# Kernel optimization log

Measured on AMD Instinct MI355X. Metric: run time of the kernel, lower is better.

The kernel has to match this reference:

```python
import jax, jax.numpy as jnp
import numpy as np

B, T, C = 4, 2048, 1024
N_HEAD = 16
HEAD_DIM = C // N_HEAD

def setup_inputs() -> dict:
    key = jax.random.key(0)
    k1, k2, k3, k4, k5 = jax.random.split(key, 5)
    sigma = (1.0 / C) ** 0.5  # encoder_var=1 default
    return {
        "x": jax.random.normal(k1, (B, T, C), dtype=jnp.float32),
        "W_attn": jax.random.normal(k2, (3 * C, C), dtype=jnp.float32) * sigma,
        "b_attn": jax.random.normal(k3, (3 * C,), dtype=jnp.float32),
        "W_proj": jax.random.normal(k4, (C, C), dtype=jnp.float32) * sigma,
        "b_proj": jax.random.normal(k5, (C,), dtype=jnp.float32),
    }

def reference(x, W_attn, b_attn, W_proj, b_proj):
    Bq, Tq, Cq = x.shape
    qkv = x @ W_attn.T + b_attn              # [B,T,3C]
    q, k, v = jnp.split(qkv, 3, axis=-1)
    def to_heads(t):
        return t.reshape(Bq, Tq, N_HEAD, HEAD_DIM).transpose(0, 2, 1, 3)  # [B,H,T,D]
    q, k, v = to_heads(q), to_heads(k), to_heads(v)
    # NOTE: original scales by 1/head_dim (not 1/sqrt(head_dim))
    att = jnp.einsum('bhqd,bhkd->bhqk', q, k) * (1.0 / HEAD_DIM)
    causal = jnp.tril(jnp.ones((Tq, Tq), dtype=bool))
    att = jnp.where(causal[None, None], att, -jnp.inf)
    att = jax.nn.softmax(att, axis=-1)
    y = jnp.einsum('bhqk,bhkd->bhqd', att, v)
    y = y.transpose(0, 2, 1, 3).reshape(Bq, Tq, Cq)
    return y @ W_proj.T + b_proj
```

## Files before the change

kernel.cpp:

```cpp
#include <hip/hip_runtime.h>

typedef __attribute__((ext_vector_type(8))) short s16x8;
typedef __attribute__((ext_vector_type(4))) float f32x4;
typedef __attribute__((ext_vector_type(4))) unsigned short u16x4;

#define T_  2048
#define C_  1024
#define D_  64

__device__ __forceinline__ unsigned short f2bf(float f){
  union { float fv; unsigned int u; } v; v.fv = f;
  unsigned int r = v.u + 0x7FFFu + ((v.u >> 16) & 1u);
  return (unsigned short)(r >> 16);
}

__device__ __forceinline__ float exp2_asm(float x){
  float r; asm("v_exp_f32 %0, %1" : "=v"(r) : "v"(x)); return r;
}
__device__ __forceinline__ unsigned int cvtpk(float lo, float hi){
  unsigned int r; asm("v_cvt_pk_bf16_f32 %0, %1, %2" : "=v"(r) : "v"(lo), "v"(hi)); return r;
}

__device__ __forceinline__ void gload_lds16(const void* g, void* l){
  __builtin_amdgcn_global_load_lds(
      (const __attribute__((address_space(1))) unsigned int*)g,
      (__attribute__((address_space(3))) unsigned int*)l, 16, 0, 0);
}

__global__ __launch_bounds__(256) void cvt_kernel(const float* __restrict__ src,
                                                  unsigned short* __restrict__ dst){
  size_t i = ((size_t)blockIdx.x * 256u + threadIdx.x) * 8u;
  f32x4 a = *(const f32x4*)(src + i);
  f32x4 b = *(const f32x4*)(src + i + 4);
  s16x8 o;
  #pragma unroll
  for (int j = 0; j < 4; ++j){ o[j] = (short)f2bf(a[j]); o[4+j] = (short)f2bf(b[j]); }
  *(s16x8*)(dst + i) = o;
}

template<int MODE>
__global__ __launch_bounds__(256, 2) void gemm_bt(
    const unsigned short* __restrict__ A, const unsigned short* __restrict__ Bw,
    const float* __restrict__ bias, int M, int N, int K, int nbx,
    unsigned short* __restrict__ q_ws, unsigned short* __restrict__ k_ws,
    unsigned short* __restrict__ vT_ws, float* __restrict__ out)
{
  __shared__ unsigned short Asm[2][128*64];
  __shared__ unsigned short Bsm[2][128*64];
  const int tid = threadIdx.x;
  const int lane = tid & 63, wid = tid >> 6;
  const int g = lane >> 4, lr = lane & 15;
  const int wr = wid >> 1, wc = wid & 1;
  const int nwg = (int)gridDim.x;
  const int cpx = nwg >> 3;
  const int orig = (int)blockIdx.x;
  const int wgid = (orig & 7) * cpx + (orig >> 3);
  const int bx = wgid % nbx, by = wgid / nbx;
  const int m0 = by * 128, n0 = bx * 128;
  const int swz = (lr & 7) << 4;

  f32x4 acc[4][4];
  #pragma unroll
  for (int i = 0; i < 4; ++i)
    #pragma unroll
    for (int j = 0; j < 4; ++j) acc[i][j] = (f32x4){0.f,0.f,0.f,0.f};

  auto stage = [&](int kt, int buf){
    const int k0 = kt << 6;
    #pragma unroll
    for (int j = 0; j < 4; ++j){
      const int c = j*256 + tid;
      const int row = c >> 3, jc = c & 7;
      const int sc = (jc ^ (row & 7)) << 4;
      gload_lds16((const char*)A  + ((size_t)(m0+row)*K + k0)*2 + sc,
                  (char*)&Asm[buf][0] + (size_t)c*16);
      gload_lds16((const char*)Bw + ((size_t)(n0+row)*K + k0)*2 + sc,
                  (char*)&Bsm[buf][0] + (size_t)c*16);
    }
  };

  const int nk = K >> 6;
  stage(0, 0);
  stage(1, 1);

  for (int t = 0; t < nk; ++t){
    const int cur = t & 1;
    if (t < nk - 1) asm volatile("s_waitcnt vmcnt(8)" ::: "memory");
    else            asm volatile("s_waitcnt vmcnt(0)" ::: "memory");
    asm volatile("s_barrier" ::: "memory");

    const char* At = (const char*)&Asm[cur][0];
    const char* Bt = (const char*)&Bsm[cur][0];

    #pragma unroll
    for (int s = 0; s < 2; ++s){
      s16x8 af[4], bf[4];
      #pragma unroll
      for (int mi = 0; mi < 4; ++mi){
        const int row = wr*64 + mi*16 + lr;
        af[mi] = *(const s16x8*)(At + row*128 + ((s*64 + g*16) ^ swz));
      }
      #pragma unroll
      for (int ni = 0; ni < 4; ++ni){
        const int row = wc*64 + ni*16 + lr;
        bf[ni] = *(const s16x8*)(Bt + row*128 + ((s*64 + g*16) ^ swz));
      }
      __builtin_amdgcn_s_setprio(1);
      #pragma unroll
      for (int mi = 0; mi < 4; ++mi)
        #pragma unroll
        for (int ni = 0; ni < 4; ++ni)
          acc[mi][ni] = __builtin_amdgcn_mfma_f32_16x16x32_bf16(af[mi], bf[ni], acc[mi][ni], 0, 0, 0);
      __builtin_amdgcn_s_setprio(0);
    }

    asm volatile("s_barrier" ::: "memory");
    if (t + 2 < nk) stage(t + 2, cur);
  }

  #pragma unroll
  for (int mi = 0; mi < 4; ++mi){
    #pragma unroll
    for (int ni = 0; ni < 4; ++ni){
      const int n = n0 + wc*64 + ni*16 + lr;
      const float bv = bias[n];
      #pragma unroll
      for (int r = 0; r < 4; ++r){
        const int m = m0 + wr*64 + mi*16 + g*4 + r;
        const float val = acc[mi][ni][r] + bv;
        if (MODE == 0){
          const int which = n >> 10;
          const int cc = n & 1023;
          const int h = cc >> 6, d = cc & 63;
          const int bq = m >> 11, t = m & 2047;
          const int bh = bq*16 + h;
          if (which == 0)      q_ws[((size_t)bh*T_ + t)*D_ + d] = f2bf(val * 0.022542110013890054f);
          else if (which == 1) k_ws[((size_t)bh*T_ + t)*D_ + d] = f2bf(val);
          else                 vT_ws[((size_t)bh*D_ + d)*T_ + t] = f2bf(val);
        } else {
          out[(size_t)m*N + n] = val;
        }
      }
    }
  }
}

__global__ __launch_bounds__(256, 4) void attn_kernel(
    const unsigned short* __restrict__ q_ws, const unsigned short* __restrict__ k_ws,
    const unsigned short* __restrict__ vT_ws, unsigned short* __restrict__ y_ws)
{
  __shared__ __align__(16) unsigned short Ks[2][64*64];
  __shared__ __align__(16) unsigned short Vs[2][64*64];

  const int tid = threadIdx.x;
  const int lane = tid & 63, wid = tid >> 6;
  const int g = lane >> 4, lr = lane & 15;
  const int orig = (int)blockIdx.x;
  const int wgid = (orig & 7) * 128 + (orig >> 3);
  const int p  = wgid & 15;
  const int bh = wgid >> 4;
  const int qwA = p*64 + wid*16,  qwB = (31 - p)*64 + wid*16;
  const int qrowA = qwA + lr,     qrowB = qwB + lr;
  const int swz = (lr & 7) << 4;

  const unsigned short* Qb = q_ws  + (size_t)bh*T_*D_;
  const unsigned short* Kb = k_ws  + (size_t)bh*T_*D_;
  const unsigned short* Vb = vT_ws + (size_t)bh*D_*T_;

  auto stage = [&](int t, int buf){
    const int kt0 = t << 6;
    #pragma unroll
    for (int s = 0; s < 2; ++s){
      const int c = s*256 + tid;
      const int r = c >> 3;
      const int scol = ((c & 7) << 4) ^ ((r & 7) << 4);
      gload_lds16((const char*)Kb + ((size_t)(kt0 + r)*D_)*2 + scol,
                  (char*)&Ks[buf][0] + c*16);
      gload_lds16((const char*)Vb + ((size_t)r*T_ + kt0)*2 + scol,
                  (char*)&Vs[buf][0] + c*16);
    }
  };

  const s16x8 bqA0 = *(const s16x8*)&Qb[(size_t)(qwA+lr)*D_ + g*8];
  const s16x8 bqA1 = *(const s16x8*)&Qb[(size_t)(qwA+lr)*D_ + 32 + g*8];
  const s16x8 bqB0 = *(const s16x8*)&Qb[(size_t)(qwB+lr)*D_ + g*8];
  const s16x8 bqB1 = *(const s16x8*)&Qb[(size_t)(qwB+lr)*D_ + 32 + g*8];

  s16x8 ones;
  #pragma unroll
  for (int j = 0; j < 8; ++j) ones[j] = (short)0x3F80;

  f32x4 yA[4], yB[4];
  #pragma unroll
  for (int dt = 0; dt < 4; ++dt){ yA[dt] = (f32x4){0.f,0.f,0.f,0.f}; yB[dt] = (f32x4){0.f,0.f,0.f,0.f}; }
  f32x4 lacA = (f32x4){0.f,0.f,0.f,0.f}, lacB = (f32x4){0.f,0.f,0.f,0.f};
  float mA = -1e30f, mB = -1e30f;

  const int ntA = p + 1, ntB = 32 - p;
  stage(0, 0);
  __syncthreads();

  for (int t = 0; t < ntB; ++t){
    const int cur = t & 1;
    if (t + 1 < ntB) stage(t + 1, cur ^ 1);
    const int kt0 = t << 6;
    const unsigned short* Kt = &Ks[cur][0];
    const unsigned short* Vt = &Vs[cur][0];
    unsigned short* Pw = &Ks[cur][wid*1024];
    const bool actA = (t < ntA);

    f32x4 sB[4], sA[4];
    #pragma unroll
    for (int kk = 0; kk < 4; ++kk){
      const int row = kk*16 + lr;
      const s16x8 a0 = *(const s16x8*)&Kt[row*64 + (((g*16)      ^ swz) >> 1)];
      const s16x8 a1 = *(const s16x8*)&Kt[row*64 + (((64 + g*16) ^ swz) >> 1)];
      f32x4 acc = (f32x4){0.f,0.f,0.f,0.f};
      acc = __builtin_amdgcn_mfma_f32_16x16x32_bf16(a0, bqB0, acc, 0, 0, 0);
      acc = __builtin_amdgcn_mfma_f32_16x16x32_bf16(a1, bqB1, acc, 0, 0, 0);
      sB[kk] = acc;
      if (actA){
        f32x4 acc2 = (f32x4){0.f,0.f,0.f,0.f};
        acc2 = __builtin_amdgcn_mfma_f32_16x16x32_bf16(a0, bqA0, acc2, 0, 0, 0);
        acc2 = __builtin_amdgcn_mfma_f32_16x16x32_bf16(a1, bqA1, acc2, 0, 0, 0);
        sA[kk] = acc2;
      }
    }

    if (kt0 + 63 > qwB){
      #pragma unroll
      for (int kk = 0; kk < 4; ++kk)
        #pragma unroll
        for (int r = 0; r < 4; ++r)
          if (kt0 + kk*16 + g*4 + r > qrowB) sB[kk][r] = -1e30f;
    }
    {
      float m01 = fmaxf(fmaxf(sB[0][0], sB[0][1]), fmaxf(sB[0][2], sB[0][3]));
      float m23 = fmaxf(fmaxf(sB[1][0], sB[1][1]), fmaxf(sB[1][2], sB[1][3]));
      float m45 = fmaxf(fmaxf(sB[2][0], sB[2][1]), fmaxf(sB[2][2], sB[2][3]));
      float m67 = fmaxf(fmaxf(sB[3][0], sB[3][1]), fmaxf(sB[3][2], sB[3][3]));
      float mx = fmaxf(fmaxf(m01, m23), fmaxf(m45, m67));
      mx = fmaxf(mx, __shfl_xor(mx, 16, 64));
      mx = fmaxf(mx, __shfl_xor(mx, 32, 64));
      if (!__all(mx <= mB + 8.f)){
        const float mnew = fmaxf(mB, mx);
        const float corr = exp2_asm(mB - mnew);
        mB = mnew;
        lacB[0] *= corr;
        #pragma unroll
        for (int dt = 0; dt < 4; ++dt)
          #pragma unroll
          for (int r = 0; r < 4; ++r) yB[dt][r] *= corr;
      }
    }
    union { unsigned int u[2]; u16x4 v; } pkB[4];
    #pragma unroll
    for (int kk = 0; kk < 4; ++kk){
      const float e0 = exp2_asm(sB[kk][0] - mB);
      const float e1 = exp2_asm(sB[kk][1] - mB);
      const float e2 = exp2_asm(sB[kk][2] - mB);
      const float e3 = exp2_asm(sB[kk][3] - mB);
      pkB[kk].u[0] = cvtpk(e0, e1);
      pkB[kk].u[1] = cvtpk(e2, e3);
    }

    asm volatile("s_barrier" ::: "memory");

    #pragma unroll
    for (int kk = 0; kk < 4; ++kk)
      *(u16x4*)&Pw[lr*64 + (((kk*32 + g*8) ^ swz) >> 1)] = pkB[kk].v;
    asm volatile("" ::: "memory");
    {
      const s16x8 p0 = *(const s16x8*)&Pw[lr*64 + (((g*16)      ^ swz) >> 1)];
      const s16x8 p1 = *(const s16x8*)&Pw[lr*64 + (((64 + g*16) ^ swz) >> 1)];
      lacB = __builtin_amdgcn_mfma_f32_16x16x32_bf16(ones, p0, lacB, 0, 0, 0);
      lacB = __builtin_amdgcn_mfma_f32_16x16x32_bf16(ones, p1, lacB, 0, 0, 0);
      #pragma unroll
      for (int dt = 0; dt < 4; ++dt){
        const int vrow = dt*16 + lr;
        const s16x8 v0 = *(const s16x8*)&Vt[vrow*64 + (((g*16)      ^ swz) >> 1)];
        const s16x8 v1 = *(const s16x8*)&Vt[vrow*64 + (((64 + g*16) ^ swz) >> 1)];
        yB[dt] = __builtin_amdgcn_mfma_f32_16x16x32_bf16(v0, p0, yB[dt], 0, 0, 0);
        yB[dt] = __builtin_amdgcn_mfma_f32_16x16x32_bf16(v1, p1, yB[dt], 0, 0, 0);
      }
    }

    if (actA){
      if (kt0 + 63 > qwA){
        #pragma unroll
        for (int kk = 0; kk < 4; ++kk)
          #pragma unroll
          for (int r = 0; r < 4; ++r)
            if (kt0 + kk*16 + g*4 + r > qrowA) sA[kk][r] = -1e30f;
      }
      float m01 = fmaxf(fmaxf(sA[0][0], sA[0][1]), fmaxf(sA[0][2], sA[0][3]));
      float m23 = fmaxf(fmaxf(sA[1][0], sA[1][1]), fmaxf(sA[1][2], sA[1][3]));
      float m45 = fmaxf(fmaxf(sA[2][0], sA[2][1]), fmaxf(sA[2][2], sA[2][3]));
      float m67 = fmaxf(fmaxf(sA[3][0], sA[3][1]), fmaxf(sA[3][2], sA[3][3]));
      float mx = fmaxf(fmaxf(m01, m23), fmaxf(m45, m67));
      mx = fmaxf(mx, __shfl_xor(mx, 16, 64));
      mx = fmaxf(mx, __shfl_xor(mx, 32, 64));
      if (!__all(mx <= mA + 8.f)){
        const float mnew = fmaxf(mA, mx);
        const float corr = exp2_asm(mA - mnew);
        mA = mnew;
        lacA[0] *= corr;
        #pragma unroll
        for (int dt = 0; dt < 4; ++dt)
          #pragma unroll
          for (int r = 0; r < 4; ++r) yA[dt][r] *= corr;
      }
      union { unsigned int u[2]; u16x4 v; } pkA[4];
      #pragma unroll
      for (int kk = 0; kk < 4; ++kk){
        const float e0 = exp2_asm(sA[kk][0] - mA);
        const float e1 = exp2_asm(sA[kk][1] - mA);
        const float e2 = exp2_asm(sA[kk][2] - mA);
        const float e3 = exp2_asm(sA[kk][3] - mA);
        pkA[kk].u[0] = cvtpk(e0, e1);
        pkA[kk].u[1] = cvtpk(e2, e3);
      }
      asm volatile("" ::: "memory");
      #pragma unroll
      for (int kk = 0; kk < 4; ++kk)
        *(u16x4*)&Pw[lr*64 + (((kk*32 + g*8) ^ swz) >> 1)] = pkA[kk].v;
      asm volatile("" ::: "memory");
      const s16x8 p0 = *(const s16x8*)&Pw[lr*64 + (((g*16)      ^ swz) >> 1)];
      const s16x8 p1 = *(const s16x8*)&Pw[lr*64 + (((64 + g*16) ^ swz) >> 1)];
      lacA = __builtin_amdgcn_mfma_f32_16x16x32_bf16(ones, p0, lacA, 0, 0, 0);
      lacA = __builtin_amdgcn_mfma_f32_16x16x32_bf16(ones, p1, lacA, 0, 0, 0);
      #pragma unroll
      for (int dt = 0; dt < 4; ++dt){
        const int vrow = dt*16 + lr;
        const s16x8 v0 = *(const s16x8*)&Vt[vrow*64 + (((g*16)      ^ swz) >> 1)];
        const s16x8 v1 = *(const s16x8*)&Vt[vrow*64 + (((64 + g*16) ^ swz) >> 1)];
        yA[dt] = __builtin_amdgcn_mfma_f32_16x16x32_bf16(v0, p0, yA[dt], 0, 0, 0);
        yA[dt] = __builtin_amdgcn_mfma_f32_16x16x32_bf16(v1, p1, yA[dt], 0, 0, 0);
      }
    }

    __syncthreads();
  }

  const int bq = bh >> 4, h = bh & 15;
  {
    const float inv = 1.f / lacB[0];
    #pragma unroll
    for (int dt = 0; dt < 4; ++dt){
      union { unsigned int u[2]; u16x4 v; } w;
      w.u[0] = cvtpk(yB[dt][0]*inv, yB[dt][1]*inv);
      w.u[1] = cvtpk(yB[dt][2]*inv, yB[dt][3]*inv);
      *(u16x4*)&y_ws[((size_t)(bq*T_ + qwB + lr))*C_ + h*64 + dt*16 + g*4] = w.v;
    }
  }
  {
    const float inv = 1.f / lacA[0];
    #pragma unroll
    for (int dt = 0; dt < 4; ++dt){
      union { unsigned int u[2]; u16x4 v; } w;
      w.u[0] = cvtpk(yA[dt][0]*inv, yA[dt][1]*inv);
      w.u[1] = cvtpk(yA[dt][2]*inv, yA[dt][3]*inv);
      *(u16x4*)&y_ws[((size_t)(bq*T_ + qwA + lr))*C_ + h*64 + dt*16 + g*4] = w.v;
    }
  }
}

extern "C" void kernel_launch(void* const* d_in, const int* in_sizes, int n_in,
                              void* d_out, int out_size, void* d_ws, size_t ws_size,
                              hipStream_t stream) {
  const float* x  = (const float*)d_in[0];
  const float* Wa = (const float*)d_in[1];
  const float* ba = (const float*)d_in[2];
  const float* Wp = (const float*)d_in[3];
  const float* bp = (const float*)d_in[4];
  float* out = (float*)d_out;

  char* ws = (char*)d_ws;
  const size_t MB = 1024u*1024u;
  unsigned short* xb  = (unsigned short*)(ws + 0);
  unsigned short* wab = (unsigned short*)(ws + 16*MB);
  unsigned short* wpb = (unsigned short*)(ws + 22*MB);
  unsigned short* qws = (unsigned short*)(ws + 24*MB);
  unsigned short* kws = (unsigned short*)(ws + 40*MB);
  unsigned short* vT  = (unsigned short*)(ws + 56*MB);
  unsigned short* yws = (unsigned short*)(ws + 72*MB);

  cvt_kernel<<<4096, 256, 0, stream>>>(x,  xb);
  cvt_kernel<<<1536, 256, 0, stream>>>(Wa, wab);
  cvt_kernel<<< 512, 256, 0, stream>>>(Wp, wpb);

  gemm_bt<0><<<dim3(1536), 256, 0, stream>>>(xb, wab, ba, 8192, 3072, 1024, 24,
                                             qws, kws, vT, nullptr);
  attn_kernel<<<dim3(1024), 256, 0, stream>>>(qws, kws, vT, yws);
  gemm_bt<1><<<dim3(512), 256, 0, stream>>>(yws, wpb, bp, 8192, 1024, 1024, 8,
                                            nullptr, nullptr, nullptr, out);
}
```

Before: 195.0 us.

## Restructure GEMM into 256x128 tiles with 4-slot K=32 pipeline

The GEMM now runs 8-wave workgroups over 256x128 output tiles. Each wave still computes 64x64, and B fragments are shared across more waves. The K loop is split into 32-wide steps held in a 4-slot LDS ring with 3 stages in flight, a rotating swizzle, and a single barrier per step, with global loads issued before the MFMAs. The goal is to hide memory latency better and cut barrier overhead. In exchange there are more loop iterations with fewer MFMAs each, and fewer workgroups in the grid.

```diff
diff --git a/kernel.cpp b/kernel.cpp
--- a/kernel.cpp
+++ b/kernel.cpp
@@ -39,25 +39,24 @@
 }
 
 template<int MODE>
-__global__ __launch_bounds__(256, 2) void gemm_bt(
+__global__ __launch_bounds__(512, 2) void gemm_bt(
     const unsigned short* __restrict__ A, const unsigned short* __restrict__ Bw,
     const float* __restrict__ bias, int M, int N, int K, int nbx,
     unsigned short* __restrict__ q_ws, unsigned short* __restrict__ k_ws,
     unsigned short* __restrict__ vT_ws, float* __restrict__ out)
 {
-  __shared__ unsigned short Asm[2][128*64];
-  __shared__ unsigned short Bsm[2][128*64];
+  __shared__ unsigned short Asl[4][256*32];
+  __shared__ unsigned short Bsl[4][128*32];
   const int tid = threadIdx.x;
   const int lane = tid & 63, wid = tid >> 6;
   const int g = lane >> 4, lr = lane & 15;
-  const int wr = wid >> 1, wc = wid & 1;
+  const int wm = wid >> 1, wn = wid & 1;
   const int nwg = (int)gridDim.x;
   const int cpx = nwg >> 3;
   const int orig = (int)blockIdx.x;
   const int wgid = (orig & 7) * cpx + (orig >> 3);
   const int bx = wgid % nbx, by = wgid / nbx;
-  const int m0 = by * 128, n0 = bx * 128;
-  const int swz = (lr & 7) << 4;
+  const int m0 = by * 256, n0 = bx * 128;
 
   f32x4 acc[4][4];
   #pragma unroll
@@ -65,68 +64,80 @@
     #pragma unroll
     for (int j = 0; j < 4; ++j) acc[i][j] = (f32x4){0.f,0.f,0.f,0.f};
 
-  auto stage = [&](int kt, int buf){
-    const int k0 = kt << 6;
-    #pragma unroll
-    for (int j = 0; j < 4; ++j){
-      const int c = j*256 + tid;
-      const int row = c >> 3, jc = c & 7;
-      const int sc = (jc ^ (row & 7)) << 4;
-      gload_lds16((const char*)A  + ((size_t)(m0+row)*K + k0)*2 + sc,
-                  (char*)&Asm[buf][0] + (size_t)c*16);
-      gload_lds16((const char*)Bw + ((size_t)(n0+row)*K + k0)*2 + sc,
-                  (char*)&Bsm[buf][0] + (size_t)c*16);
+  auto stageA = [&](int ks){
+    const int slot = ks & 3;
+    const size_t kbyte = ((size_t)ks) << 6;
+    #pragma unroll
+    for (int j = 0; j < 2; ++j){
+      const int c = j*512 + tid;
+      const int row = c >> 2;
+      const int srcq = ((c & 3) - (row >> 1)) & 3;
+      gload_lds16((const char*)A + ((size_t)(m0+row)*K)*2 + kbyte + srcq*16,
+                  (char*)&Asl[slot][0] + (size_t)c*16);
     }
   };
-
-  const int nk = K >> 6;
-  stage(0, 0);
-  stage(1, 1);
-
-  for (int t = 0; t < nk; ++t){
-    const int cur = t & 1;
-    if (t < nk - 1) asm volatile("s_waitcnt vmcnt(8)" ::: "memory");
-    else            asm volatile("s_waitcnt vmcnt(0)" ::: "memory");
-    asm volatile("s_barrier" ::: "memory");
-
-    const char* At = (const char*)&Asm[cur][0];
-    const char* Bt = (const char*)&Bsm[cur][0];
-
-    #pragma unroll
-    for (int s = 0; s < 2; ++s){
-      s16x8 af[4], bf[4];
-      #pragma unroll
-      for (int mi = 0; mi < 4; ++mi){
-        const int row = wr*64 + mi*16 + lr;
-        af[mi] = *(const s16x8*)(At + row*128 + ((s*64 + g*16) ^ swz));
-      }
-      #pragma unroll
-      for (int ni = 0; ni < 4; ++ni){
-        const int row = wc*64 + ni*16 + lr;
-        bf[ni] = *(const s16x8*)(Bt + row*128 + ((s*64 + g*16) ^ swz));
-      }
-      __builtin_amdgcn_s_setprio(1);
-      #pragma unroll
-      for (int mi = 0; mi < 4; ++mi)
-        #pragma unroll
-        for (int ni = 0; ni < 4; ++ni)
-          acc[mi][ni] = __builtin_amdgcn_mfma_f32_16x16x32_bf16(af[mi], bf[ni], acc[mi][ni], 0, 0, 0);
-      __builtin_amdgcn_s_setprio(0);
-    }
-
-    asm volatile("s_barrier" ::: "memory");
-    if (t + 2 < nk) stage(t + 2, cur);
+  auto stageB = [&](int ks){
+    const int slot = ks & 3;
+    const size_t kbyte = ((size_t)ks) << 6;
+    const int c = tid;
+    const int row = c >> 2;
+    const int srcq = ((c & 3) - (row >> 1)) & 3;
+    gload_lds16((const char*)Bw + ((size_t)(n0+row)*K)*2 + kbyte + srcq*16,
+                (char*)&Bsl[slot][0] + (size_t)c*16);
+  };
+
+  const int nks = K >> 5;
+  stageA(0); stageB(0);
+  stageA(1); stageB(1);
+  stageA(2); stageB(2);
+  asm volatile("s_waitcnt vmcnt(6)" ::: "memory");
+  asm volatile("s_barrier" ::: "memory");
+
+  for (int ks = 0; ks < nks; ++ks){
+    const int slot = ks & 3;
+    const char* As = (const char*)&Asl[slot][0];
+    const char* Bs = (const char*)&Bsl[slot][0];
+
+    s16x8 af[4], bf[4];
+    #pragma unroll
+    for (int mi = 0; mi < 4; ++mi){
+      const int row = wm*64 + mi*16 + lr;
+      af[mi] = *(const s16x8*)(As + row*64 + (((g + (row >> 1)) & 3) << 4));
+    }
+    #pragma unroll
+    for (int ni = 0; ni < 4; ++ni){
+      const int row = wn*64 + ni*16 + lr;
+      bf[ni] = *(const s16x8*)(Bs + row*64 + (((g + (row >> 1)) & 3) << 4));
+    }
+
+    if (ks + 3 < nks){ stageA(ks + 3); stageB(ks + 3); }
+
+    asm volatile("s_waitcnt lgkmcnt(0)" ::: "memory");
+    __builtin_amdgcn_s_setprio(1);
+    #pragma unroll
+    for (int mi = 0; mi < 4; ++mi)
+      #pragma unroll
+      for (int ni = 0; ni < 4; ++ni)
+        acc[mi][ni] = __builtin_amdgcn_mfma_f32_16x16x32_bf16(af[mi], bf[ni], acc[mi][ni], 0, 0, 0);
+    __builtin_amdgcn_s_setprio(0);
+
+    if (ks + 1 < nks){
+      if (ks + 3 < nks)      asm volatile("s_waitcnt vmcnt(6)" ::: "memory");
+      else if (ks + 2 < nks) asm volatile("s_waitcnt vmcnt(3)" ::: "memory");
+      else                   asm volatile("s_waitcnt vmcnt(0)" ::: "memory");
+      asm volatile("s_barrier" ::: "memory");
+    }
   }
 
   #pragma unroll
   for (int mi = 0; mi < 4; ++mi){
     #pragma unroll
     for (int ni = 0; ni < 4; ++ni){
-      const int n = n0 + wc*64 + ni*16 + lr;
+      const int n = n0 + wn*64 + ni*16 + lr;
       const float bv = bias[n];
       #pragma unroll
       for (int r = 0; r < 4; ++r){
-        const int m = m0 + wr*64 + mi*16 + g*4 + r;
+        const int m = m0 + wm*64 + mi*16 + g*4 + r;
         const float val = acc[mi][ni][r] + bv;
         if (MODE == 0){
           const int which = n >> 10;
@@ -389,9 +400,9 @@
   cvt_kernel<<<1536, 256, 0, stream>>>(Wa, wab);
   cvt_kernel<<< 512, 256, 0, stream>>>(Wp, wpb);
 
-  gemm_bt<0><<<dim3(1536), 256, 0, stream>>>(xb, wab, ba, 8192, 3072, 1024, 24,
-                                             qws, kws, vT, nullptr);
+  gemm_bt<0><<<dim3(768), 512, 0, stream>>>(xb, wab, ba, 8192, 3072, 1024, 24,
+                                            qws, kws, vT, nullptr);
   attn_kernel<<<dim3(1024), 256, 0, stream>>>(qws, kws, vT, yws);
-  gemm_bt<1><<<dim3(512), 256, 0, stream>>>(yws, wpb, bp, 8192, 1024, 1024, 8,
+  gemm_bt<1><<<dim3(256), 512, 0, stream>>>(yws, wpb, bp, 8192, 1024, 1024, 8,
                                             nullptr, nullptr, nullptr, out);
 }
```

New measurement: 198.4 us. About the same (+1.7%).

## Load GEMM B operand directly from global into registers instead of LDS

Applied to the files above, without the earlier changes.

The GEMM kernel no longer stages the weight (B) tile through shared memory. Each wave now loads its B fragments straight from global memory into registers, with one k-step of register prefetch, while the A tile stays double-buffered in LDS. Halving LDS use is meant to let three workgroups share a CU instead of two and to remove the LDS reads for B. The cost is that each of the two waves sharing a column block loads the same B data from global/L2, plus higher register pressure and vmcnt accounting that depends on the compiler emitting loads in the expected order.

```diff
diff --git a/kernel.cpp b/kernel.cpp
--- a/kernel.cpp
+++ b/kernel.cpp
@@ -39,14 +39,13 @@
 }
 
 template<int MODE>
-__global__ __launch_bounds__(256, 2) void gemm_bt(
+__global__ __launch_bounds__(256, 3) void gemm_bt(
     const unsigned short* __restrict__ A, const unsigned short* __restrict__ Bw,
     const float* __restrict__ bias, int M, int N, int K, int nbx,
     unsigned short* __restrict__ q_ws, unsigned short* __restrict__ k_ws,
     unsigned short* __restrict__ vT_ws, float* __restrict__ out)
 {
   __shared__ unsigned short Asm[2][128*64];
-  __shared__ unsigned short Bsm[2][128*64];
   const int tid = threadIdx.x;
   const int lane = tid & 63, wid = tid >> 6;
   const int g = lane >> 4, lr = lane & 15;
@@ -65,57 +64,82 @@
     #pragma unroll
     for (int j = 0; j < 4; ++j) acc[i][j] = (f32x4){0.f,0.f,0.f,0.f};
 
-  auto stage = [&](int kt, int buf){
-    const int k0 = kt << 6;
+  auto stageA = [&](int kt, int buf){
     #pragma unroll
     for (int j = 0; j < 4; ++j){
       const int c = j*256 + tid;
       const int row = c >> 3, jc = c & 7;
       const int sc = (jc ^ (row & 7)) << 4;
-      gload_lds16((const char*)A  + ((size_t)(m0+row)*K + k0)*2 + sc,
+      gload_lds16((const char*)A + ((size_t)(m0+row)*K)*2 + (size_t)kt*128 + sc,
                   (char*)&Asm[buf][0] + (size_t)c*16);
-      gload_lds16((const char*)Bw + ((size_t)(n0+row)*K + k0)*2 + sc,
-                  (char*)&Bsm[buf][0] + (size_t)c*16);
     }
   };
 
+  const unsigned short* bptr0 = Bw + (size_t)(n0 + wc*64 +  0 + lr)*K + g*8;
+  const unsigned short* bptr1 = Bw + (size_t)(n0 + wc*64 + 16 + lr)*K + g*8;
+  const unsigned short* bptr2 = Bw + (size_t)(n0 + wc*64 + 32 + lr)*K + g*8;
+  const unsigned short* bptr3 = Bw + (size_t)(n0 + wc*64 + 48 + lr)*K + g*8;
+
+  s16x8 Bp[4], Bq[4];
   const int nk = K >> 6;
-  stage(0, 0);
-  stage(1, 1);
+
+  stageA(0, 0);
+  Bp[0] = *(const s16x8*)(bptr0); Bp[1] = *(const s16x8*)(bptr1);
+  Bp[2] = *(const s16x8*)(bptr2); Bp[3] = *(const s16x8*)(bptr3);
+  Bq[0] = *(const s16x8*)(bptr0+32); Bq[1] = *(const s16x8*)(bptr1+32);
+  Bq[2] = *(const s16x8*)(bptr2+32); Bq[3] = *(const s16x8*)(bptr3+32);
+  stageA(1, 1);
 
   for (int t = 0; t < nk; ++t){
     const int cur = t & 1;
-    if (t < nk - 1) asm volatile("s_waitcnt vmcnt(8)" ::: "memory");
-    else            asm volatile("s_waitcnt vmcnt(0)" ::: "memory");
+    if (t < nk - 1) asm volatile("s_waitcnt vmcnt(12)" ::: "memory");
+    else            asm volatile("s_waitcnt vmcnt(8)"  ::: "memory");
     asm volatile("s_barrier" ::: "memory");
 
     const char* At = (const char*)&Asm[cur][0];
-    const char* Bt = (const char*)&Bsm[cur][0];
-
-    #pragma unroll
-    for (int s = 0; s < 2; ++s){
-      s16x8 af[4], bf[4];
+    const size_t koff = (size_t)(t + 1) * 64;
+
+    {
+      s16x8 af[4];
       #pragma unroll
       for (int mi = 0; mi < 4; ++mi){
         const int row = wr*64 + mi*16 + lr;
-        af[mi] = *(const s16x8*)(At + row*128 + ((s*64 + g*16) ^ swz));
-      }
-      #pragma unroll
-      for (int ni = 0; ni < 4; ++ni){
-        const int row = wc*64 + ni*16 + lr;
-        bf[ni] = *(const s16x8*)(Bt + row*128 + ((s*64 + g*16) ^ swz));
+        af[mi] = *(const s16x8*)(At + row*128 + ((g*16) ^ swz));
       }
       __builtin_amdgcn_s_setprio(1);
       #pragma unroll
       for (int mi = 0; mi < 4; ++mi)
         #pragma unroll
         for (int ni = 0; ni < 4; ++ni)
-          acc[mi][ni] = __builtin_amdgcn_mfma_f32_16x16x32_bf16(af[mi], bf[ni], acc[mi][ni], 0, 0, 0);
+          acc[mi][ni] = __builtin_amdgcn_mfma_f32_16x16x32_bf16(af[mi], Bp[ni], acc[mi][ni], 0, 0, 0);
       __builtin_amdgcn_s_setprio(0);
+      if (t + 1 < nk){
+        Bp[0] = *(const s16x8*)(bptr0 + koff); Bp[1] = *(const s16x8*)(bptr1 + koff);
+        Bp[2] = *(const s16x8*)(bptr2 + koff); Bp[3] = *(const s16x8*)(bptr3 + koff);
+      }
+    }
+    {
+      s16x8 af[4];
+      #pragma unroll
+      for (int mi = 0; mi < 4; ++mi){
+        const int row = wr*64 + mi*16 + lr;
+        af[mi] = *(const s16x8*)(At + row*128 + ((64 + g*16) ^ swz));
+      }
+      __builtin_amdgcn_s_setprio(1);
+      #pragma unroll
+      for (int mi = 0; mi < 4; ++mi)
+        #pragma unroll
+        for (int ni = 0; ni < 4; ++ni)
+          acc[mi][ni] = __builtin_amdgcn_mfma_f32_16x16x32_bf16(af[mi], Bq[ni], acc[mi][ni], 0, 0, 0);
+      __builtin_amdgcn_s_setprio(0);
+      if (t + 1 < nk){
+        Bq[0] = *(const s16x8*)(bptr0 + koff + 32); Bq[1] = *(const s16x8*)(bptr1 + koff + 32);
+        Bq[2] = *(const s16x8*)(bptr2 + koff + 32); Bq[3] = *(const s16x8*)(bptr3 + koff + 32);
+      }
     }
 
     asm volatile("s_barrier" ::: "memory");
-    if (t + 2 < nk) stage(t + 2, cur);
+    if (t + 2 < nk) stageA(t + 2, cur);
   }
 
   #pragma unroll
```

Result: slower. 251.8 us (+29.1%).
